# Optimization experiments

Hardware: AMD Instinct MI355X
Metric: run time of the kernel (lower is better)

## Reference

```python
import jax, jax.numpy as jnp
import numpy as np

NEG = -1000000.0  # mask fill value used by the torch module


def setup_inputs() -> dict:
    key = jax.random.key(0)
    kq, kk, kv, km = jax.random.split(key, 4)
    B, Q, K, D = 8, 2048, 2048, 128
    queries = jax.random.normal(kq, (B, Q, D), dtype=jnp.float32)
    keys = jax.random.normal(kk, (B, K, D), dtype=jnp.float32)
    values = jax.random.normal(kv, (B, K, D), dtype=jnp.float32)
    attntion_mask = jax.random.randint(km, (B, K), 0, 2, dtype=jnp.int32)
    return {"queries": queries, "keys": keys, "values": values,
            "attntion_mask": attntion_mask}


def reference(queries, keys, values, attntion_mask):
    d = queries.shape[-1]
    # scores: [B, Q, K]
    scores = jnp.einsum('bqd,bkd->bqk', queries, keys) / jnp.sqrt(
        jnp.asarray(d, dtype=queries.dtype))
    # 2D mask [B, K] broadcasts over the query axis (torch repeat_interleave)
    mask = attntion_mask.astype(bool)[:, None, :]  # [B, 1, K]
    scores = jnp.where(mask, scores, NEG)
    weights = jax.nn.softmax(scores, axis=-1)
    # dropout rate is 0.0 (eval mode) -> identity
    return jnp.einsum('bqk,bkv->bqv', weights, values)
```

## Files before the change

kernel.cpp:

```cpp
#include <hip/hip_runtime.h>
#include <stdint.h>

typedef __attribute__((ext_vector_type(8))) short short8;
typedef __attribute__((ext_vector_type(4))) float f32x4;

#define NB 8
#define NQ 2048
#define NK 2048
#define ND 128
#define SCALE 0.08838834764831845f
#define L2E   1.4426950408889634f
#define FMAXC 10.0f

__device__ __forceinline__ uint32_t pk_bf16(float a, float b) {
  uint32_t ua = __builtin_bit_cast(uint32_t, a);
  uint32_t ub = __builtin_bit_cast(uint32_t, b);
  ua += 0x7FFFu + ((ua >> 16) & 1u);
  ub += 0x7FFFu + ((ub >> 16) & 1u);
  return (ua >> 16) | (ub & 0xFFFF0000u);
}

__device__ __forceinline__ void dma16(const void* g, void* l) {
  __builtin_amdgcn_global_load_lds((const __attribute__((address_space(1))) void*)g,
                                   (__attribute__((address_space(3))) void*)l, 16, 0, 0);
}

__global__ __launch_bounds__(256) void compact_kernel(const int* __restrict__ maskm,
                                                      int* __restrict__ idxArr,
                                                      int* __restrict__ KcArr) {
  __shared__ int cnt;
  const int b = blockIdx.x;
  const int t = threadIdx.x;
  const int lane = t & 63;
  if (t == 0) cnt = 0;
  __syncthreads();
#pragma unroll
  for (int j = 0; j < 8; ++j) {
    int k = t * 8 + j;
    bool bit = maskm[b * NK + k] != 0;
    unsigned long long m = __ballot(bit);
    int pre = __popcll(m & ((1ull << lane) - 1ull));
    int tot = __popcll(m);
    int base = 0;
    if (lane == 0 && tot) base = atomicAdd(&cnt, tot);
    base = __shfl(base, 0);
    if (bit) idxArr[b * NK + base + pre] = k;
  }
  __syncthreads();
  int kc = cnt;
  for (int s = kc + t; s < NK; s += 256) idxArr[b * NK + s] = -1;
  if (t == 0) KcArr[b] = kc;
}

__global__ __launch_bounds__(256) void prep_kernel(const float* __restrict__ v,
                                                   const float* __restrict__ kin,
                                                   ushort* __restrict__ vt,
                                                   ushort* __restrict__ kb,
                                                   const int* __restrict__ idxArr) {
  const int t = threadIdx.x;
  const int bid = blockIdx.x;
  if (bid < 512) {
    __shared__ __align__(16) float tile[4096];
    char* sm = (char*)tile;
    const int b = bid >> 6;
    const int k0 = ((bid >> 1) & 31) << 6;
    const int d0 = (bid & 1) << 6;
#pragma unroll
    for (int i = 0; i < 4; ++i) {
      int id = i * 256 + t;
      int k = id >> 4, c = id & 15;
      int src = idxArr[b * NK + k0 + k];
      uint4 val; val.x = 0u; val.y = 0u; val.z = 0u; val.w = 0u;
      if (src >= 0) val = *(const uint4*)(v + (size_t)(b * NK + src) * ND + d0 + c * 4);
      *(uint4*)(sm + k * 256 + ((c ^ (k & 15)) * 16)) = val;
    }
    __syncthreads();
#pragma unroll
    for (int i = 0; i < 2; ++i) {
      int id = i * 256 + t;
      int d = id >> 3, kc = id & 7;
      uint32_t w[4];
#pragma unroll
      for (int jj = 0; jj < 4; ++jj) {
        int kA = kc * 8 + jj * 2, kB = kA + 1;
        float fa = *(const float*)(sm + kA * 256 + (((d >> 2) ^ (kA & 15)) * 16) + (d & 3) * 4);
        float fb = *(const float*)(sm + kB * 256 + (((d >> 2) ^ (kB & 15)) * 16) + (d & 3) * 4);
        w[jj] = pk_bf16(fa, fb);
      }
      uint4 o; o.x = w[0]; o.y = w[1]; o.z = w[2]; o.w = w[3];
      *(uint4*)(vt + (size_t)(b * ND + d0 + d) * NK + k0 + kc * 8) = o;
    }
  } else {
    int gs = (bid - 512) * 16 + (t >> 4);
    int src = idxArr[gs];
    int col = (t & 15) * 8;
    uint4 u; u.x = 0u; u.y = 0u; u.z = 0u; u.w = 0u;
    if (src >= 0) {
      int b2 = gs >> 11;
      const float* p = kin + (size_t)(b2 * NK + src) * ND + col;
      f32x4 a = *(const f32x4*)p;
      f32x4 c = *(const f32x4*)(p + 4);
      u.x = pk_bf16(a[0], a[1]); u.y = pk_bf16(a[2], a[3]);
      u.z = pk_bf16(c[0], c[1]); u.w = pk_bf16(c[2], c[3]);
    }
    *(uint4*)(kb + (size_t)gs * ND + col) = u;
  }
}

template <bool MASKED>
__device__ __forceinline__ void do_softmax(const f32x4 st[2], float& l_,
                                           char* pbase, int r, int quad, int rem) {
  const float C1 = SCALE * L2E;
  const float C2 = -FMAXC * L2E;
  float p[2][4]; float ps = 0.f;
#pragma unroll
  for (int mt = 0; mt < 2; ++mt) {
    float t0 = fmaf(st[mt][0], C1, C2);
    float t1 = fmaf(st[mt][1], C1, C2);
    float t2 = fmaf(st[mt][2], C1, C2);
    float t3 = fmaf(st[mt][3], C1, C2);
    if (MASKED) {
      const int rm = rem - mt * 16;
      t0 = (rm > 0) ? t0 : -2.0e6f;
      t1 = (rm > 1) ? t1 : -2.0e6f;
      t2 = (rm > 2) ? t2 : -2.0e6f;
      t3 = (rm > 3) ? t3 : -2.0e6f;
    }
    p[mt][0] = exp2f(t0); p[mt][1] = exp2f(t1);
    p[mt][2] = exp2f(t2); p[mt][3] = exp2f(t3);
    ps += p[mt][0] + p[mt][1] + p[mt][2] + p[mt][3];
  }
  l_ += ps;
#pragma unroll
  for (int mt = 0; mt < 2; ++mt) {
    uint2 w; w.x = pk_bf16(p[mt][0], p[mt][1]); w.y = pk_bf16(p[mt][2], p[mt][3]);
    *(uint2*)(pbase + r * 64 + (((mt * 4 + quad) ^ (r & 6)) * 8)) = w;
  }
}

#define LDS_BYTES 73728
__global__ __launch_bounds__(512) void attn_kernel(const float* __restrict__ qm,
                                                   const ushort* __restrict__ kbm,
                                                   const ushort* __restrict__ vtm,
                                                   const int* __restrict__ KcArr,
                                                   ushort* __restrict__ opart,
                                                   float* __restrict__ lpart) {
  __shared__ __align__(16) char sm[LDS_BYTES];
  const int o   = blockIdx.x;
  const int bid = (o & 7) * 64 + (o >> 3);
  const int b   = bid >> 6;
  const int q0  = ((bid >> 2) & 15) << 7;
  const int spl = bid & 3;
  const int t = threadIdx.x;
  const int lane = t & 63;
  const int wave = t >> 6;
  const int r = lane & 15;
  const int quad = lane >> 4;
  const int half = wave >> 2;
  const int qg = wave & 3;

  const int Kc   = KcArr[b];
  const int n_it = (Kc + 255) >> 8;
  const int CH   = n_it << 5;

  uint32_t koff[2], voff[2];
#pragma unroll
  for (int j = 0; j < 2; ++j) {
    int i = wave * 2 + j;
    int rho = i * 4 + (lane >> 4);
    int ck = (lane & 15) ^ (rho & 15);
    int krow = (spl * 2 + (rho >> 5)) * CH + (rho & 31);
    koff[j] = (uint32_t)(b * NK + krow) * ND + ck * 8;
    int rv = i * 16 + (lane >> 2);
    int cv = (lane & 3) ^ (rv & 3);
    voff[j] = (uint32_t)(b * ND + (rv & 127)) * NK + (spl * 2 + (rv >> 7)) * CH + cv * 8;
  }

#pragma unroll
  for (int j = 0; j < 2; ++j) {
    dma16(kbm + koff[j], sm + (wave * 2 + j) * 1024);
    dma16(vtm + voff[j], sm + 32768 + (wave * 2 + j) * 1024);
  }

  short8 qf[2][4];
#pragma unroll
  for (int qt = 0; qt < 2; ++qt)
#pragma unroll
    for (int ks = 0; ks < 4; ++ks) {
      const float* p = qm + (size_t)(b * NQ + q0 + qg * 32 + qt * 16 + r) * ND + ks * 32 + quad * 8;
      f32x4 a = *(const f32x4*)p;
      f32x4 c = *(const f32x4*)(p + 4);
      uint4 u;
      u.x = pk_bf16(a[0], a[1]); u.y = pk_bf16(a[2], a[3]);
      u.z = pk_bf16(c[0], c[1]); u.w = pk_bf16(c[2], c[3]);
      qf[qt][ks] = __builtin_bit_cast(short8, u);
    }

  f32x4 oacc[2][8];
#pragma unroll
  for (int qt = 0; qt < 2; ++qt)
#pragma unroll
    for (int dt = 0; dt < 8; ++dt) oacc[qt][dt] = (f32x4){0.f, 0.f, 0.f, 0.f};
  float l_[2] = {0.f, 0.f};

  char* const pbase = sm + 65536 + wave * 1024;

  const int vlim0 = Kc - (spl * 2 + half) * CH;

  for (int it = 0; it < n_it; ++it) {
    const int cur = it & 1;
    char* const kcur = sm + cur * 16384;
    char* const knxt = sm + (cur ^ 1) * 16384;
    char* const vcur = sm + 32768 + cur * 16384;
    char* const vnxt = sm + 32768 + (cur ^ 1) * 16384;

    __syncthreads();

    if (it < n_it - 1) {
      const uint32_t kadd = (uint32_t)(it + 1) * 32 * ND;
      const uint32_t vadd = (uint32_t)(it + 1) * 32;
#pragma unroll
      for (int j = 0; j < 2; ++j) {
        dma16(kbm + koff[j] + kadd, knxt + (wave * 2 + j) * 1024);
        dma16(vtm + voff[j] + vadd, vnxt + (wave * 2 + j) * 1024);
      }
    }

    f32x4 st[2][2];
#pragma unroll
    for (int mt = 0; mt < 2; ++mt) {
      short8 kf[4];
#pragma unroll
      for (int ks = 0; ks < 4; ++ks)
        kf[ks] = *(const short8*)(kcur + half * 8192 + (mt * 16 + r) * 256 + (((ks * 4 + quad) ^ r) * 16));
#pragma unroll
      for (int qt = 0; qt < 2; ++qt) {
        f32x4 acc = (f32x4){0.f, 0.f, 0.f, 0.f};
#pragma unroll
        for (int ks = 0; ks < 4; ++ks)
          acc = __builtin_amdgcn_mfma_f32_16x16x32_bf16(kf[ks], qf[qt][ks], acc, 0, 0, 0);
        st[mt][qt] = acc;
      }
    }

    const int vlim = vlim0 - it * 32;
    short8 pf[2];
#pragma unroll
    for (int qt = 0; qt < 2; ++qt) {
      f32x4 s2[2] = { st[0][qt], st[1][qt] };
      if (vlim >= 32) do_softmax<false>(s2, l_[qt], pbase, r, quad, 0);
      else            do_softmax<true >(s2, l_[qt], pbase, r, quad, vlim - quad * 4);
      pf[qt] = *(const short8*)(pbase + r * 64 + (((quad * 2) ^ (r & 6)) * 8));
    }

#pragma unroll
    for (int dt = 0; dt < 8; ++dt) {
      short8 vf = *(const short8*)(vcur + half * 8192 + (dt * 16 + r) * 64 + ((quad ^ (r & 3)) * 16));
#pragma unroll
      for (int qt = 0; qt < 2; ++qt)
        oacc[qt][dt] = __builtin_amdgcn_mfma_f32_16x16x32_bf16(vf, pf[qt], oacc[qt][dt], 0, 0, 0);
    }
  }

  __syncthreads();
  float* xch = (float*)(sm + qg * 17408) + lane * 68;
  if (half == 1) {
    xch[0] = l_[0]; xch[1] = l_[1];
#pragma unroll
    for (int qt = 0; qt < 2; ++qt)
#pragma unroll
      for (int dt = 0; dt < 8; ++dt)
        *(f32x4*)(xch + 4 + (qt * 8 + dt) * 4) = oacc[qt][dt];
  }
  __syncthreads();
  if (half == 0) {
#pragma unroll
    for (int qt = 0; qt < 2; ++qt) {
      const int qrow = b * NQ + q0 + qg * 32 + qt * 16 + r;
      float ls = l_[qt] + xch[qt];
      ls += __shfl_xor(ls, 16);
      ls += __shfl_xor(ls, 32);
      if (quad == 0) lpart[spl * NB * NQ + qrow] = ls;
#pragma unroll
      for (int dt = 0; dt < 8; ++dt) {
        f32x4 o1 = *(const f32x4*)(xch + 4 + (qt * 8 + dt) * 4);
        f32x4 ov = oacc[qt][dt] + o1;
        uint2 w; w.x = pk_bf16(ov[0], ov[1]); w.y = pk_bf16(ov[2], ov[3]);
        *(uint2*)(opart + (size_t)spl * NB * NQ * ND + (size_t)qrow * ND + dt * 16 + quad * 4) = w;
      }
    }
  }
}

__global__ __launch_bounds__(256) void merge_kernel(const ushort* __restrict__ opart,
                                                    const float* __restrict__ lpart,
                                                    float* __restrict__ outm) {
  const int gid = blockIdx.x * 256 + threadIdx.x;
  const int row = gid >> 4;
  const int d0 = (gid & 15) << 3;
  const size_t off = (size_t)row * ND + d0;
  float acc[8];
#pragma unroll
  for (int j = 0; j < 8; ++j) acc[j] = 0.f;
  float lsum = 0.f;
#pragma unroll
  for (int s = 0; s < 4; ++s) {
    uint4 u = *(const uint4*)(opart + (size_t)s * NB * NQ * ND + off);
    lsum += lpart[s * NB * NQ + row];
    acc[0] += __builtin_bit_cast(float, u.x << 16);
    acc[1] += __builtin_bit_cast(float, u.x & 0xFFFF0000u);
    acc[2] += __builtin_bit_cast(float, u.y << 16);
    acc[3] += __builtin_bit_cast(float, u.y & 0xFFFF0000u);
    acc[4] += __builtin_bit_cast(float, u.z << 16);
    acc[5] += __builtin_bit_cast(float, u.z & 0xFFFF0000u);
    acc[6] += __builtin_bit_cast(float, u.w << 16);
    acc[7] += __builtin_bit_cast(float, u.w & 0xFFFF0000u);
  }
  float inv = 1.0f / lsum;
  f32x4 lo, hi;
  lo[0] = acc[0] * inv; lo[1] = acc[1] * inv; lo[2] = acc[2] * inv; lo[3] = acc[3] * inv;
  hi[0] = acc[4] * inv; hi[1] = acc[5] * inv; hi[2] = acc[6] * inv; hi[3] = acc[7] * inv;
  *(f32x4*)(outm + off) = lo;
  *(f32x4*)(outm + off + 4) = hi;
}

extern "C" void kernel_launch(void* const* d_in, const int* in_sizes, int n_in,
                              void* d_out, int out_size, void* d_ws, size_t ws_size,
                              hipStream_t stream) {
  const float* q   = (const float*)d_in[0];
  const float* k   = (const float*)d_in[1];
  const float* v   = (const float*)d_in[2];
  const int*   msk = (const int*)d_in[3];
  float* out = (float*)d_out;
  ushort* kb = (ushort*)d_ws;
  ushort* vt = kb + (size_t)NB * NK * ND;
  ushort* op = vt + (size_t)NB * NK * ND;
  float*  lp = (float*)(op + 4 * (size_t)NB * NQ * ND);
  int* idxA  = (int*)(lp + 4 * (size_t)NB * NQ);
  int* kcA   = idxA + (size_t)NB * NK;

  compact_kernel<<<NB, 256, 0, stream>>>(msk, idxA, kcA);
  prep_kernel<<<1536, 256, 0, stream>>>(v, k, vt, kb, idxA);
  attn_kernel<<<512, 512, 0, stream>>>(q, kb, vt, kcA, op, lp);
  merge_kernel<<<1024, 256, 0, stream>>>(op, lp, out);
}
```

Baseline: 114.7 us.

## Halve key splits, triple-buffer K/V tiles, and simplify two-way merge

The key dimension is now split 2 ways instead of 4, so the attention kernel launches 256 blocks that each iterate over twice as many tiles. The K/V LDS ring grows from double to triple buffering: two tiles are prefetched ahead, guarded by explicit vmcnt waits and raw barriers, and the Q global loads are issued before the first DMA. The merge kernel and workspace layout shrink to two partials, which cuts partial-output traffic. The trade-off is lower grid parallelism (256 blocks on a 256-CU part) and more LDS per block.

```diff
diff --git a/kernel.cpp b/kernel.cpp
--- a/kernel.cpp
+++ b/kernel.cpp
@@ -138,7 +138,7 @@
   }
 }
 
-#define LDS_BYTES 73728
+#define LDS_BYTES 106496
 __global__ __launch_bounds__(512) void attn_kernel(const float* __restrict__ qm,
                                                    const ushort* __restrict__ kbm,
                                                    const ushort* __restrict__ vtm,
@@ -147,10 +147,10 @@
                                                    float* __restrict__ lpart) {
   __shared__ __align__(16) char sm[LDS_BYTES];
   const int o   = blockIdx.x;
-  const int bid = (o & 7) * 64 + (o >> 3);
-  const int b   = bid >> 6;
-  const int q0  = ((bid >> 2) & 15) << 7;
-  const int spl = bid & 3;
+  const int bid = (o & 7) * 32 + (o >> 3);
+  const int b   = bid >> 5;
+  const int q0  = ((bid >> 1) & 15) << 7;
+  const int spl = bid & 1;
   const int t = threadIdx.x;
   const int lane = t & 63;
   const int wave = t >> 6;
@@ -160,7 +160,7 @@
   const int qg = wave & 3;
 
   const int Kc   = KcArr[b];
-  const int n_it = (Kc + 255) >> 8;
+  const int n_it = (Kc + 127) >> 7;
   const int CH   = n_it << 5;
 
   uint32_t koff[2], voff[2];
@@ -176,23 +176,40 @@
     voff[j] = (uint32_t)(b * ND + (rv & 127)) * NK + (spl * 2 + (rv >> 7)) * CH + cv * 8;
   }
 
-#pragma unroll
-  for (int j = 0; j < 2; ++j) {
-    dma16(kbm + koff[j], sm + (wave * 2 + j) * 1024);
-    dma16(vtm + voff[j], sm + 32768 + (wave * 2 + j) * 1024);
-  }
-
-  short8 qf[2][4];
+#define ISSUE_TILE(tt, bufi)                                                    \
+  {                                                                             \
+    const uint32_t kadd_ = (uint32_t)(tt) * 32 * ND;                            \
+    const uint32_t vadd_ = (uint32_t)(tt) * 32;                                 \
+    char* kb_ = sm + (bufi) * 16384;                                            \
+    char* vb_ = sm + 49152 + (bufi) * 16384;                                    \
+    _Pragma("unroll")                                                           \
+    for (int j = 0; j < 2; ++j) {                                               \
+      dma16(kbm + koff[j] + kadd_, kb_ + (wave * 2 + j) * 1024);                \
+      dma16(vtm + voff[j] + vadd_, vb_ + (wave * 2 + j) * 1024);                \
+    }                                                                           \
+  }
+
+  f32x4 qraw[2][4][2];
 #pragma unroll
   for (int qt = 0; qt < 2; ++qt)
 #pragma unroll
     for (int ks = 0; ks < 4; ++ks) {
       const float* p = qm + (size_t)(b * NQ + q0 + qg * 32 + qt * 16 + r) * ND + ks * 32 + quad * 8;
-      f32x4 a = *(const f32x4*)p;
-      f32x4 c = *(const f32x4*)(p + 4);
+      qraw[qt][ks][0] = *(const f32x4*)p;
+      qraw[qt][ks][1] = *(const f32x4*)(p + 4);
+    }
+  ISSUE_TILE(0, 0);
+  if (n_it > 1) ISSUE_TILE(1, 1);
+  short8 qf[2][4];
+#pragma unroll
+  for (int qt = 0; qt < 2; ++qt)
+#pragma unroll
+    for (int ks = 0; ks < 4; ++ks) {
       uint4 u;
-      u.x = pk_bf16(a[0], a[1]); u.y = pk_bf16(a[2], a[3]);
-      u.z = pk_bf16(c[0], c[1]); u.w = pk_bf16(c[2], c[3]);
+      u.x = pk_bf16(qraw[qt][ks][0][0], qraw[qt][ks][0][1]);
+      u.y = pk_bf16(qraw[qt][ks][0][2], qraw[qt][ks][0][3]);
+      u.z = pk_bf16(qraw[qt][ks][1][0], qraw[qt][ks][1][1]);
+      u.w = pk_bf16(qraw[qt][ks][1][2], qraw[qt][ks][1][3]);
       qf[qt][ks] = __builtin_bit_cast(short8, u);
     }
 
@@ -203,28 +220,25 @@
     for (int dt = 0; dt < 8; ++dt) oacc[qt][dt] = (f32x4){0.f, 0.f, 0.f, 0.f};
   float l_[2] = {0.f, 0.f};
 
-  char* const pbase = sm + 65536 + wave * 1024;
+  char* const pbase = sm + 98304 + wave * 1024;
 
   const int vlim0 = Kc - (spl * 2 + half) * CH;
 
+  int cur = 0;
   for (int it = 0; it < n_it; ++it) {
-    const int cur = it & 1;
+    if (it < n_it - 1) asm volatile("s_waitcnt vmcnt(4)" ::: "memory");
+    else               asm volatile("s_waitcnt vmcnt(0)" ::: "memory");
+    __builtin_amdgcn_sched_barrier(0);
+    __builtin_amdgcn_s_barrier();
+    __builtin_amdgcn_sched_barrier(0);
+
+    if (it + 2 < n_it) {
+      int b2 = cur + 2; if (b2 >= 3) b2 -= 3;
+      ISSUE_TILE(it + 2, b2);
+    }
+
     char* const kcur = sm + cur * 16384;
-    char* const knxt = sm + (cur ^ 1) * 16384;
-    char* const vcur = sm + 32768 + cur * 16384;
-    char* const vnxt = sm + 32768 + (cur ^ 1) * 16384;
-
-    __syncthreads();
-
-    if (it < n_it - 1) {
-      const uint32_t kadd = (uint32_t)(it + 1) * 32 * ND;
-      const uint32_t vadd = (uint32_t)(it + 1) * 32;
-#pragma unroll
-      for (int j = 0; j < 2; ++j) {
-        dma16(kbm + koff[j] + kadd, knxt + (wave * 2 + j) * 1024);
-        dma16(vtm + voff[j] + vadd, vnxt + (wave * 2 + j) * 1024);
-      }
-    }
+    char* const vcur = sm + 49152 + cur * 16384;
 
     f32x4 st[2][2];
 #pragma unroll
@@ -260,6 +274,8 @@
       for (int qt = 0; qt < 2; ++qt)
         oacc[qt][dt] = __builtin_amdgcn_mfma_f32_16x16x32_bf16(vf, pf[qt], oacc[qt][dt], 0, 0, 0);
     }
+
+    cur = (cur == 2) ? 0 : cur + 1;
   }
 
   __syncthreads();
@@ -290,6 +306,7 @@
       }
     }
   }
+#undef ISSUE_TILE
 }
 
 __global__ __launch_bounds__(256) void merge_kernel(const ushort* __restrict__ opart,
@@ -299,27 +316,19 @@
   const int row = gid >> 4;
   const int d0 = (gid & 15) << 3;
   const size_t off = (size_t)row * ND + d0;
-  float acc[8];
-#pragma unroll
-  for (int j = 0; j < 8; ++j) acc[j] = 0.f;
-  float lsum = 0.f;
-#pragma unroll
-  for (int s = 0; s < 4; ++s) {
-    uint4 u = *(const uint4*)(opart + (size_t)s * NB * NQ * ND + off);
-    lsum += lpart[s * NB * NQ + row];
-    acc[0] += __builtin_bit_cast(float, u.x << 16);
-    acc[1] += __builtin_bit_cast(float, u.x & 0xFFFF0000u);
-    acc[2] += __builtin_bit_cast(float, u.y << 16);
-    acc[3] += __builtin_bit_cast(float, u.y & 0xFFFF0000u);
-    acc[4] += __builtin_bit_cast(float, u.z << 16);
-    acc[5] += __builtin_bit_cast(float, u.z & 0xFFFF0000u);
-    acc[6] += __builtin_bit_cast(float, u.w << 16);
-    acc[7] += __builtin_bit_cast(float, u.w & 0xFFFF0000u);
-  }
-  float inv = 1.0f / lsum;
+  uint4 u0 = *(const uint4*)(opart + off);
+  uint4 u1 = *(const uint4*)(opart + (size_t)NB * NQ * ND + off);
+  float inv = 1.0f / (lpart[row] + lpart[NB * NQ + row]);
   f32x4 lo, hi;
-  lo[0] = acc[0] * inv; lo[1] = acc[1] * inv; lo[2] = acc[2] * inv; lo[3] = acc[3] * inv;
-  hi[0] = acc[4] * inv; hi[1] = acc[5] * inv; hi[2] = acc[6] * inv; hi[3] = acc[7] * inv;
+  uint32_t w;
+#define UP(u, dst0, dst1) w = (u); dst0 = __builtin_bit_cast(float, w << 16); \
+                          dst1 = __builtin_bit_cast(float, w & 0xFFFF0000u);
+  float a0,a1,b0,b1;
+  UP(u0.x, a0, a1) UP(u1.x, b0, b1) lo[0] = (a0 + b0) * inv; lo[1] = (a1 + b1) * inv;
+  UP(u0.y, a0, a1) UP(u1.y, b0, b1) lo[2] = (a0 + b0) * inv; lo[3] = (a1 + b1) * inv;
+  UP(u0.z, a0, a1) UP(u1.z, b0, b1) hi[0] = (a0 + b0) * inv; hi[1] = (a1 + b1) * inv;
+  UP(u0.w, a0, a1) UP(u1.w, b0, b1) hi[2] = (a0 + b0) * inv; hi[3] = (a1 + b1) * inv;
+#undef UP
   *(f32x4*)(outm + off) = lo;
   *(f32x4*)(outm + off + 4) = hi;
 }
@@ -335,12 +344,12 @@
   ushort* kb = (ushort*)d_ws;
   ushort* vt = kb + (size_t)NB * NK * ND;
   ushort* op = vt + (size_t)NB * NK * ND;
-  float*  lp = (float*)(op + 4 * (size_t)NB * NQ * ND);
-  int* idxA  = (int*)(lp + 4 * (size_t)NB * NQ);
+  float*  lp = (float*)(op + 2 * (size_t)NB * NQ * ND);
+  int* idxA  = (int*)(lp + 2 * (size_t)NB * NQ);
   int* kcA   = idxA + (size_t)NB * NK;
 
   compact_kernel<<<NB, 256, 0, stream>>>(msk, idxA, kcA);
   prep_kernel<<<1536, 256, 0, stream>>>(v, k, vt, kb, idxA);
-  attn_kernel<<<512, 512, 0, stream>>>(q, kb, vt, kcA, op, lp);
+  attn_kernel<<<256, 512, 0, stream>>>(q, kb, vt, kcA, op, lp);
   merge_kernel<<<1024, 256, 0, stream>>>(op, lp, out);
 }
```

Result: faster. 107.0 us (-6.7%).
